# Performance work log

Measured on AMD Instinct MI355X. Metric: run time of the kernel, lower is better.

Reference implementation:

```python
import math
import jax, jax.numpy as jnp
import numpy as np

DIM = 1024
QK_DIM = 200
HIDDEN = 2 * DIM  # expansion_factor = 2
N = 8192


def setup_inputs() -> dict:
    key = jax.random.key(0)
    ks = jax.random.split(key, 8)
    s = 0.02
    return {
        "x": jax.random.normal(ks[0], (N, DIM), dtype=jnp.float32),
        "W_hidden": jax.random.normal(ks[1], (DIM, 2 * HIDDEN), dtype=jnp.float32) * s,
        "b_hidden": jnp.zeros((2 * HIDDEN,), dtype=jnp.float32),
        "W_qk": jax.random.normal(ks[2], (DIM, QK_DIM), dtype=jnp.float32) * s,
        "b_qk": jnp.zeros((QK_DIM,), dtype=jnp.float32),
        "gamma": 1.0 + jax.random.normal(ks[3], (2, QK_DIM), dtype=jnp.float32) * s,
        "beta": jnp.zeros((2, QK_DIM), dtype=jnp.float32),
        "W_out": jax.random.normal(ks[4], (HIDDEN, DIM), dtype=jnp.float32) * s,
        "b_out": jnp.zeros((DIM,), dtype=jnp.float32),
    }


def reference(x, W_hidden, b_hidden, W_qk, b_qk, gamma, beta, W_out, b_out):
    # to_hidden: Linear(dim -> 2*hidden) + SiLU, then chunk into v, gate
    hid = jax.nn.silu(x @ W_hidden + b_hidden)        # [N, 2H]
    v, gate = jnp.split(hid, 2, axis=-1)              # [N, H] each
    # to_qk: Linear(dim -> qk_dim) + SiLU
    qk = jax.nn.silu(x @ W_qk + b_qk)                 # [N, qk]
    # OffsetScale (heads=2): per-head affine on the shared qk
    q = qk * gamma[0] + beta[0]                       # [N, qk]
    k = qk * gamma[1] + beta[1]                       # [N, qk]
    # scores scaled by sqrt(dim) (module uses self.dim, not qk_dim)
    sim = (q @ k.T) * (1.0 / math.sqrt(x.shape[-1]))  # [N, N]
    # ReLU-squared attention (no softmax); dropout=0.0 -> identity
    attn = jnp.square(jax.nn.relu(sim))
    out = attn @ v                                    # [N, H]
    out = out * gate
    out = out @ W_out + b_out                         # [N, dim]
    # add_residual=True in this module multiplies by x
    return out * x
```

## Files before the change

### kernel.cpp

```cpp
#include <hip/hip_runtime.h>
#include <stdint.h>


typedef __bf16 bf16x8 __attribute__((ext_vector_type(8)));
typedef float f32x4 __attribute__((ext_vector_type(4)));

__device__ __forceinline__ uint16_t f2bf(float f) {
  uint32_t u = __builtin_bit_cast(uint32_t, f);
  u += 0x7fffu + ((u >> 16) & 1u);
  return (uint16_t)(u >> 16);
}
__device__ __forceinline__ float silu_f(float s) {
  return s / (1.f + __expf(-s));
}

__device__ __forceinline__ void gload16(const void* g, void* l) {
  __builtin_amdgcn_global_load_lds(
      (__attribute__((address_space(1))) void*)const_cast<void*>(g),
      (__attribute__((address_space(3))) void*)l, 16, 0, 0);
}


__global__ void cast_to_bf16(const float* __restrict__ in, uint16_t* __restrict__ out, int n4) {
  int i = blockIdx.x * blockDim.x + threadIdx.x;
  if (i < n4) {
    float4 f = ((const float4*)in)[i];
    ushort4 o;
    o.x = f2bf(f.x); o.y = f2bf(f.y); o.z = f2bf(f.z); o.w = f2bf(f.w);
    ((ushort4*)out)[i] = o;
  }
}

__global__ void transpose_cast_pad(const float* __restrict__ in, uint16_t* __restrict__ out,
                                   int R, int C, int Cp) {
  __shared__ float tile[32][33];
  int cb = blockIdx.x * 32;
  int rb = blockIdx.y * 32;
  int tx = threadIdx.x;
  int ty = threadIdx.y;
#pragma unroll
  for (int i = 0; i < 4; ++i) {
    int r = rb + ty + i * 8;
    int c = cb + tx;
    tile[ty + i * 8][tx] = (c < C) ? in[(size_t)r * C + c] : 0.f;
  }
  __syncthreads();
#pragma unroll
  for (int i = 0; i < 4; ++i) {
    int c = cb + ty + i * 8;
    if (c < Cp) out[(size_t)c * R + rb + tx] = f2bf(tile[tx][ty + i * 8]);
  }
}


struct EpiParams {
  const float* bias;
  const float* bias2;
  const float* g0;
  const float* b0;
  const float* g1;
  const float* b1;
  const uint16_t* gate;
  const float* x;
  uint16_t* o16a;
  uint16_t* o16b;
  uint16_t* oq;
  uint16_t* ok;
  float* o32;
};

#define TILE128(T_, B_, BS_)                                                   \
  do {                                                                         \
    const uint16_t* base_ = SH + (B_) * 8192;                                  \
    const int kp_ = (((T_) + 3) & (NT - 1)) * 32;                              \
    uint16_t* sd_ = SH + (BS_) * 8192 + wave * 512;                            \
    gload16(gA0 + kp_, sd_);                                                   \
    gload16(gA1 + kp_, sd_ + 2048);                                            \
    gload16(gB0 + kp_, sd_ + 4096);                                            \
    gload16(gB1 + kp_, sd_ + 6144);                                            \
    bf16x8 a_[4], b_[4];                                                       \
    _Pragma("unroll") for (int j = 0; j < 4; ++j)                              \
        b_[j] = *(const bf16x8*)(base_ + rdB + j * 512);                       \
    _Pragma("unroll") for (int i = 0; i < 4; ++i)                              \
        a_[i] = *(const bf16x8*)(base_ + rdA + i * 512);                       \
    __builtin_amdgcn_s_setprio(1);                                             \
    _Pragma("unroll") for (int i = 0; i < 4; ++i)                              \
      _Pragma("unroll") for (int j = 0; j < 4; ++j)                            \
          acc[i][j] = __builtin_amdgcn_mfma_f32_16x16x32_bf16(                 \
              a_[i], b_[j], acc[i][j], 0, 0, 0);                               \
    __builtin_amdgcn_s_setprio(0);                                             \
    asm volatile("s_waitcnt vmcnt(8)" ::: "memory");                           \
    __builtin_amdgcn_sched_barrier(0);                                         \
    __builtin_amdgcn_s_barrier();                                              \
    __builtin_amdgcn_sched_barrier(0);                                         \
  } while (0)

#define RING_LOOP128()                                                         \
  do {                                                                         \
    _Pragma("unroll") for (int s_ = 0; s_ < 3; ++s_) {                         \
      uint16_t* d_ = SH + s_ * 8192 + wave * 512;                              \
      gload16(gA0 + s_ * 32, d_);                                              \
      gload16(gA1 + s_ * 32, d_ + 2048);                                       \
      gload16(gB0 + s_ * 32, d_ + 4096);                                       \
      gload16(gB1 + s_ * 32, d_ + 6144);                                       \
    }                                                                          \
    asm volatile("s_waitcnt vmcnt(8)" ::: "memory");                           \
    __builtin_amdgcn_sched_barrier(0);                                         \
    __builtin_amdgcn_s_barrier();                                              \
    __builtin_amdgcn_sched_barrier(0);                                         \
    for (int t0_ = 0; t0_ < NT; t0_ += 4) {                                    \
      TILE128(t0_ + 0, 0, 3);                                                  \
      TILE128(t0_ + 1, 1, 0);                                                  \
      TILE128(t0_ + 2, 2, 1);                                                  \
      TILE128(t0_ + 3, 3, 2);                                                  \
    }                                                                          \
    asm volatile("s_waitcnt vmcnt(0)" ::: "memory");                           \
    __builtin_amdgcn_sched_barrier(0);                                         \
    __syncthreads();                                                           \
  } while (0)

__global__ __launch_bounds__(256, 2) void k_hidqk(
    const uint16_t* __restrict__ A, const uint16_t* __restrict__ Bt, EpiParams p) {
  __shared__ __align__(16) uint16_t SH[32768];

  const int tid = threadIdx.x;
  const int lane = tid & 63;
  const int wave = tid >> 6;
  const int wr = (wave >> 1) * 64;
  const int wc = (wave & 1) * 64;
  const int m0 = blockIdx.y * 128;
  const int n0 = blockIdx.x * 128;
  const int lda = 1024, ldb = 1024;
  const int NT = 32;

  f32x4 acc[4][4] = {};

  const int fr = lane & 15;
  const int rg = lane >> 4;
  const int swz = (rg ^ ((fr >> 1) & 3)) * 8;
  const int rdA = (wr + fr) * 32 + swz;
  const int rdB = 4096 + (wc + fr) * 32 + swz;

  const int srow = lane >> 2;
  const int sk = ((lane & 3) ^ ((lane >> 3) & 3)) * 8;
  const uint16_t* gA0 = A + (size_t)(m0 + wave * 16 + srow) * lda + sk;
  const uint16_t* gA1 = gA0 + (size_t)64 * lda;
  const uint16_t* gB0 = Bt + (size_t)(n0 + wave * 16 + srow) * ldb + sk;
  const uint16_t* gB1 = gB0 + (size_t)64 * ldb;

  RING_LOOP128();

  if (n0 < 2048) {
    uint16_t* ar = SH + wave * 2048;
    const int lrow = lane >> 3;
    const int mc = (lane & 7) * 8;
#pragma unroll
    for (int j = 0; j < 4; ++j) {
      const float bc = p.bias[n0 + wc + j * 16 + fr];
#pragma unroll
      for (int i = 0; i < 4; ++i)
#pragma unroll
        for (int r = 0; r < 4; ++r)
          ar[fr * 72 + i * 16 + rg * 4 + r] = f2bf(silu_f(acc[i][j][r] + bc));
#pragma unroll
      for (int rr = 0; rr < 2; ++rr) {
        bf16x8 v = *(const bf16x8*)(ar + (rr * 8 + lrow) * 72 + mc);
        *(bf16x8*)(p.o16a + (size_t)(n0 + wc + j * 16 + rr * 8 + lrow) * 8192 + m0 + wr + mc) = v;
      }
    }
  } else if (n0 < 4096) {
    uint16_t* ar = SH + wave * 2048;
    const int lrow = lane >> 3;
    const int nc = (lane & 7) * 8;
    float bc[4];
#pragma unroll
    for (int j = 0; j < 4; ++j) bc[j] = p.bias[n0 + wc + j * 16 + fr];
#pragma unroll
    for (int i = 0; i < 4; ++i) {
#pragma unroll
      for (int j = 0; j < 4; ++j)
#pragma unroll
        for (int r = 0; r < 4; ++r)
          ar[(rg * 4 + r) * 72 + j * 16 + fr] = f2bf(silu_f(acc[i][j][r] + bc[j]));
#pragma unroll
      for (int rr = 0; rr < 2; ++rr) {
        bf16x8 v = *(const bf16x8*)(ar + (rr * 8 + lrow) * 72 + nc);
        *(bf16x8*)(p.o16b + (size_t)(m0 + wr + i * 16 + rr * 8 + lrow) * 2048 + (n0 - 2048) + wc + nc) = v;
      }
    }
  } else {
#pragma unroll
    for (int i = 0; i < 4; ++i) {
#pragma unroll
      for (int j = 0; j < 4; ++j) {
        const int row = m0 + wr + i * 16 + rg * 4;
        const int qc = n0 + wc + j * 16 + fr - 4096;
#pragma unroll
        for (int r = 0; r < 4; ++r) {
          float qv = 0.f, kv = 0.f;
          if (qc < 200) {
            float s = silu_f(acc[i][j][r] + p.bias2[qc]);
            qv = s * p.g0[qc] + p.b0[qc];
            kv = s * p.g1[qc] + p.b1[qc];
          }
          p.oq[(size_t)(row + r) * 256 + qc] = f2bf(qv);
          p.ok[(size_t)(row + r) * 256 + qc] = f2bf(kv);
        }
      }
    }
  }
}

__global__ __launch_bounds__(256, 2) void k_attn(
    const uint16_t* __restrict__ Q,
    const uint16_t* __restrict__ Kt,
    uint16_t* __restrict__ attn) {
  __shared__ __align__(16) uint16_t SH[32768];

  const int tid = threadIdx.x;
  const int lane = tid & 63;
  const int wave = tid >> 6;
  const int wr = (wave >> 1) * 64;
  const int wc = (wave & 1) * 64;
  const int m0 = blockIdx.y * 128;
  const int n0 = blockIdx.x * 128;
  const int lda = 256, ldb = 256;
  const int NT = 8;

  f32x4 acc[4][4] = {};

  const int fr = lane & 15;
  const int rg = lane >> 4;
  const int swz = (rg ^ ((fr >> 1) & 3)) * 8;
  const int rdA = (wr + fr) * 32 + swz;
  const int rdB = 4096 + (wc + fr) * 32 + swz;

  const int srow = lane >> 2;
  const int sk = ((lane & 3) ^ ((lane >> 3) & 3)) * 8;
  const uint16_t* gA0 = Q + (size_t)(m0 + wave * 16 + srow) * lda + sk;
  const uint16_t* gA1 = gA0 + (size_t)64 * lda;
  const uint16_t* gB0 = Kt + (size_t)(n0 + wave * 16 + srow) * ldb + sk;
  const uint16_t* gB1 = gB0 + (size_t)64 * ldb;

  RING_LOOP128();

#pragma unroll
  for (int i = 0; i < 4; ++i) {
    uint16_t* sl = SH + wave * 4096 + (i & 1) * 2048;
#pragma unroll
    for (int j = 0; j < 4; ++j)
#pragma unroll
      for (int r = 0; r < 4; ++r) {
        float s = fmaxf(acc[i][j][r] * 0.03125f, 0.f);
        sl[(rg * 4 + r) * 72 + j * 16 + fr] = f2bf(s * s);
      }
    const int row = lane >> 2;
    const int c0 = (lane & 3) * 16;
    bf16x8 v0 = *(const bf16x8*)(sl + row * 72 + c0);
    bf16x8 v1 = *(const bf16x8*)(sl + row * 72 + c0 + 8);
    uint16_t* dst = attn + (size_t)(m0 + wr + i * 16 + row) * 8192 + (n0 + wc + c0);
    *(bf16x8*)(dst) = v0;
    *(bf16x8*)(dst + 8) = v1;
  }
}

__global__ __launch_bounds__(512, 2) void k_pv(
    const uint16_t* __restrict__ A, int lda,
    const uint16_t* __restrict__ Bt, int ldb,
    int K, int nx, EpiParams p) {
  __shared__ __align__(16) uint16_t SH[65536];

  const int id = blockIdx.x;
  const int bx = (id >> 3) % nx;
  const int by = (id & 7) + 8 * (id / (8 * nx));
  const int m0 = by * 256;
  const int n0 = bx * 256;

  const int tid = threadIdx.x;
  const int lane = tid & 63;
  const int wave = tid >> 6;
  const int wrM = (wave >> 2) * 128;
  const int wcN = (wave & 3) * 64;

  const int fr = lane & 15;
  const int rg = lane >> 4;
  const int swz = (rg ^ ((fr >> 1) & 3)) * 8;

  const int rdA = (wrM + fr) * 32 + swz;
  const int rdB = 8192 + (wcN + fr) * 32 + swz;

  const int srow = lane >> 2;
  const int sk = ((lane & 3) ^ ((lane >> 3) & 3)) * 8;
  const uint16_t* gA0 = A + (size_t)(m0 + wave * 16 + srow) * lda + sk;
  const uint16_t* gA1 = gA0 + (size_t)128 * lda;
  const uint16_t* gB0 = Bt + (size_t)(n0 + wave * 16 + srow) * ldb + sk;
  const uint16_t* gB1 = gB0 + (size_t)128 * ldb;

  f32x4 acc[8][4] = {};
  const int NT = K >> 5;

  for (int s = 0; s < 3; ++s) {
    const int ko = s * 32;
    uint16_t* d = SH + s * 16384 + wave * 512;
    gload16(gA0 + ko, d);
    gload16(gA1 + ko, d + 4096);
    gload16(gB0 + ko, d + 8192);
    gload16(gB1 + ko, d + 12288);
  }
  asm volatile("s_waitcnt vmcnt(8)" ::: "memory");
  __builtin_amdgcn_sched_barrier(0);
  __builtin_amdgcn_s_barrier();
  __builtin_amdgcn_sched_barrier(0);

#define PV_TILE(T_, B_, BS_)                                                   \
  do {                                                                         \
    const uint16_t* bA_ = SH + (B_) * 16384;                                   \
    const int kp_ = (((T_) + 3) & (NT - 1)) * 32;                              \
    uint16_t* sd_ = SH + (BS_) * 16384 + wave * 512;                           \
    gload16(gA0 + kp_, sd_);                                                   \
    gload16(gA1 + kp_, sd_ + 4096);                                            \
    gload16(gB0 + kp_, sd_ + 8192);                                            \
    gload16(gB1 + kp_, sd_ + 12288);                                           \
    bf16x8 aq[8], bq[4];                                                       \
    _Pragma("unroll") for (int j = 0; j < 4; ++j)                              \
        bq[j] = *(const bf16x8*)(bA_ + rdB + j * 512);                         \
    _Pragma("unroll") for (int i = 0; i < 8; ++i)                              \
        aq[i] = *(const bf16x8*)(bA_ + rdA + i * 512);                         \
    __builtin_amdgcn_s_setprio(1);                                             \
    _Pragma("unroll") for (int i = 0; i < 8; ++i)                              \
      _Pragma("unroll") for (int j = 0; j < 4; ++j)                            \
          acc[i][j] = __builtin_amdgcn_mfma_f32_16x16x32_bf16(                 \
              aq[i], bq[j], acc[i][j], 0, 0, 0);                               \
    __builtin_amdgcn_s_setprio(0);                                             \
    asm volatile("s_waitcnt vmcnt(8)" ::: "memory");                           \
    __builtin_amdgcn_sched_barrier(0);                                         \
    __builtin_amdgcn_s_barrier();                                              \
    __builtin_amdgcn_sched_barrier(0);                                         \
  } while (0)

  for (int t0 = 0; t0 < NT; t0 += 4) {
    PV_TILE(t0 + 0, 0, 3);
    PV_TILE(t0 + 1, 1, 0);
    PV_TILE(t0 + 2, 2, 1);
    PV_TILE(t0 + 3, 3, 2);
  }
#undef PV_TILE

  asm volatile("s_waitcnt vmcnt(0)" ::: "memory");
  __builtin_amdgcn_sched_barrier(0);
  __builtin_amdgcn_s_barrier();
  __builtin_amdgcn_sched_barrier(0);

  uint16_t* ar = SH + wave * 2048;
  const int lrow = lane >> 3;
  const int nc = (lane & 7) * 8;
#pragma unroll
  for (int i = 0; i < 8; ++i) {
#pragma unroll
    for (int j = 0; j < 4; ++j)
#pragma unroll
      for (int r = 0; r < 4; ++r)
        ar[(rg * 4 + r) * 72 + j * 16 + fr] = f2bf(acc[i][j][r]);
#pragma unroll
    for (int rr = 0; rr < 2; ++rr) {
      const size_t base = (size_t)(m0 + wrM + i * 16 + rr * 8 + lrow) * 2048 + n0 + wcN + nc;
      bf16x8 v = *(const bf16x8*)(ar + (rr * 8 + lrow) * 72 + nc);
      bf16x8 g = *(const bf16x8*)(p.gate + base);
      bf16x8 o;
#pragma unroll
      for (int e = 0; e < 8; ++e) o[e] = (__bf16)((float)v[e] * (float)g[e]);
      *(bf16x8*)(p.o16a + base) = o;
    }
  }
}

__global__ __launch_bounds__(256, 2) void k_final(
    const uint16_t* __restrict__ A,
    const uint16_t* __restrict__ Bt, EpiParams p) {
  __shared__ __align__(16) uint16_t SH[32768];

  const int tid = threadIdx.x;
  const int lane = tid & 63;
  const int wave = tid >> 6;
  const int wr = (wave >> 1) * 64;
  const int wc = (wave & 1) * 64;
  const int m0 = blockIdx.y * 128;
  const int n0 = blockIdx.x * 128;
  const int lda = 2048, ldb = 2048;
  const int NT = 64;

  f32x4 acc[4][4] = {};

  const int fr = lane & 15;
  const int rg = lane >> 4;
  const int swz = (rg ^ ((fr >> 1) & 3)) * 8;
  const int rdA = (wr + fr) * 32 + swz;
  const int rdB = 4096 + (wc + fr) * 32 + swz;

  const int srow = lane >> 2;
  const int sk = ((lane & 3) ^ ((lane >> 3) & 3)) * 8;
  const uint16_t* gA0 = A + (size_t)(m0 + wave * 16 + srow) * lda + sk;
  const uint16_t* gA1 = gA0 + (size_t)64 * lda;
  const uint16_t* gB0 = Bt + (size_t)(n0 + wave * 16 + srow) * ldb + sk;
  const uint16_t* gB1 = gB0 + (size_t)64 * ldb;

  RING_LOOP128();

#pragma unroll
  for (int i = 0; i < 4; ++i) {
#pragma unroll
    for (int j = 0; j < 4; ++j) {
      const int row = m0 + wr + i * 16 + rg * 4;
      const int col = n0 + wc + j * 16 + fr;
      const float bc = p.bias[col];
#pragma unroll
      for (int r = 0; r < 4; ++r) {
        size_t idx = (size_t)(row + r) * 1024 + col;
        p.o32[idx] = (acc[i][j][r] + bc) * p.x[idx];
      }
    }
  }
}


extern "C" void kernel_launch(void* const* d_in, const int* in_sizes, int n_in,
                              void* d_out, int out_size, void* d_ws, size_t ws_size,
                              hipStream_t stream) {
  const float* x        = (const float*)d_in[0];
  const float* W_hidden = (const float*)d_in[1];
  const float* b_hidden = (const float*)d_in[2];
  const float* W_qk     = (const float*)d_in[3];
  const float* b_qk     = (const float*)d_in[4];
  const float* gamma    = (const float*)d_in[5];
  const float* beta     = (const float*)d_in[6];
  const float* W_out    = (const float*)d_in[7];
  const float* b_out    = (const float*)d_in[8];
  float* out = (float*)d_out;

  const bool fullM = ws_size >= (236ull << 20);
  const size_t region0 = fullM ? (128ull << 20) : (64ull << 20);

  char* base = (char*)d_ws;
  uint16_t* xb    = (uint16_t*)(base);
  uint16_t* WhT   = (uint16_t*)(base + (16ull << 20));
  uint16_t* WqkT  = (uint16_t*)(base + (24ull << 20));
  uint16_t* attnB = (uint16_t*)(base);
  char* tail = base + region0;
  uint16_t* WoT   = (uint16_t*)(tail);
  uint16_t* q     = (uint16_t*)(tail + (4ull << 20));
  uint16_t* kk    = (uint16_t*)(tail + (8ull << 20));
  uint16_t* vT    = (uint16_t*)(tail + (12ull << 20));
  uint16_t* gate  = (uint16_t*)(tail + (44ull << 20));
  uint16_t* out2g = (uint16_t*)(tail + (76ull << 20));
  (void)in_sizes; (void)n_in; (void)out_size;

  cast_to_bf16<<<(8192 * 1024 / 4) / 256, 256, 0, stream>>>(x, xb, 8192 * 1024 / 4);
  transpose_cast_pad<<<dim3(4096 / 32, 1024 / 32), dim3(32, 8), 0, stream>>>(W_hidden, WhT, 1024, 4096, 4096);
  transpose_cast_pad<<<dim3(256 / 32, 1024 / 32), dim3(32, 8), 0, stream>>>(W_qk, WqkT, 1024, 200, 256);
  transpose_cast_pad<<<dim3(1024 / 32, 2048 / 32), dim3(32, 8), 0, stream>>>(W_out, WoT, 2048, 1024, 1024);

  {
    EpiParams p{};
    p.bias = b_hidden; p.bias2 = b_qk;
    p.g0 = gamma; p.b0 = beta; p.g1 = gamma + 200; p.b1 = beta + 200;
    p.o16a = vT; p.o16b = gate; p.oq = q; p.ok = kk;
    k_hidqk<<<dim3(34, 64), 256, 0, stream>>>(xb, WhT, p);
  }

  if (fullM) {
    k_attn<<<dim3(64, 64), 256, 0, stream>>>(q, kk, attnB);
    {
      EpiParams p{};
      p.gate = gate; p.o16a = out2g;
      k_pv<<<dim3(8 * 32), 512, 0, stream>>>(attnB, 8192, vT, 8192, 8192, 8, p);
    }
  } else {
    for (int s = 0; s < 2; ++s) {
      k_attn<<<dim3(64, 32), 256, 0, stream>>>(q + (size_t)s * 4096 * 256, kk, attnB);
      {
        EpiParams p{};
        p.gate = gate + (size_t)s * 4096 * 2048;
        p.o16a = out2g + (size_t)s * 4096 * 2048;
        k_pv<<<dim3(8 * 16), 512, 0, stream>>>(attnB, 8192, vT, 8192, 8192, 8, p);
      }
    }
  }

  {
    EpiParams p{};
    p.bias = b_out; p.x = x; p.o32 = out;
    k_final<<<dim3(8, 64), 256, 0, stream>>>(out2g, WoT, p);
  }
}
```

Baseline: 570.5 us.

## Halve PV tile M to 128 and double-buffer LDS fragment reads in registers

```diff
diff --git a/kernel.cpp b/kernel.cpp
--- a/kernel.cpp
+++ b/kernel.cpp
@@ -268,18 +268,18 @@
     const uint16_t* __restrict__ A, int lda,
     const uint16_t* __restrict__ Bt, int ldb,
     int K, int nx, EpiParams p) {
-  __shared__ __align__(16) uint16_t SH[65536];
+  __shared__ __align__(16) uint16_t SH[49152];
 
   const int id = blockIdx.x;
   const int bx = (id >> 3) % nx;
   const int by = (id & 7) + 8 * (id / (8 * nx));
-  const int m0 = by * 256;
+  const int m0 = by * 128;
   const int n0 = bx * 256;
 
   const int tid = threadIdx.x;
   const int lane = tid & 63;
   const int wave = tid >> 6;
-  const int wrM = (wave >> 2) * 128;
+  const int wrM = (wave >> 2) * 64;
   const int wcN = (wave & 3) * 64;
 
   const int fr = lane & 15;
@@ -287,64 +287,67 @@
   const int swz = (rg ^ ((fr >> 1) & 3)) * 8;
 
   const int rdA = (wrM + fr) * 32 + swz;
-  const int rdB = 8192 + (wcN + fr) * 32 + swz;
+  const int rdB = 4096 + (wcN + fr) * 32 + swz;
 
   const int srow = lane >> 2;
   const int sk = ((lane & 3) ^ ((lane >> 3) & 3)) * 8;
   const uint16_t* gA0 = A + (size_t)(m0 + wave * 16 + srow) * lda + sk;
-  const uint16_t* gA1 = gA0 + (size_t)128 * lda;
-  const uint16_t* gB0 = Bt + (size_t)(n0 + wave * 16 + srow) * ldb + sk;
-  const uint16_t* gB1 = gB0 + (size_t)128 * ldb;
-
-  f32x4 acc[8][4] = {};
+  const uint16_t* gB0 = Bt + (size_t)(n0 + wave * 32 + srow) * ldb + sk;
+  const uint16_t* gB1 = gB0 + (size_t)16 * ldb;
+
+  f32x4 acc[4][4] = {};
   const int NT = K >> 5;
 
   for (int s = 0; s < 3; ++s) {
     const int ko = s * 32;
-    uint16_t* d = SH + s * 16384 + wave * 512;
-    gload16(gA0 + ko, d);
-    gload16(gA1 + ko, d + 4096);
-    gload16(gB0 + ko, d + 8192);
-    gload16(gB1 + ko, d + 12288);
-  }
-  asm volatile("s_waitcnt vmcnt(8)" ::: "memory");
+    uint16_t* d = SH + s * 12288;
+    gload16(gA0 + ko, d + wave * 512);
+    gload16(gB0 + ko, d + 4096 + wave * 1024);
+    gload16(gB1 + ko, d + 4096 + wave * 1024 + 512);
+  }
+  asm volatile("s_waitcnt vmcnt(3)" ::: "memory");
   __builtin_amdgcn_sched_barrier(0);
   __builtin_amdgcn_s_barrier();
   __builtin_amdgcn_sched_barrier(0);
 
-#define PV_TILE(T_, B_, BS_)                                                   \
+  bf16x8 fa0[4], fb0[4], fa1[4], fb1[4];
+#pragma unroll
+  for (int j = 0; j < 4; ++j) fb0[j] = *(const bf16x8*)(SH + rdB + j * 512);
+#pragma unroll
+  for (int i = 0; i < 4; ++i) fa0[i] = *(const bf16x8*)(SH + rdA + i * 512);
+
+#define PV_T(T_, RS_, WS_, CA_, CB_, NA_, NB_)                                 \
   do {                                                                         \
-    const uint16_t* bA_ = SH + (B_) * 16384;                                   \
     const int kp_ = (((T_) + 3) & (NT - 1)) * 32;                              \
-    uint16_t* sd_ = SH + (BS_) * 16384 + wave * 512;                           \
-    gload16(gA0 + kp_, sd_);                                                   \
-    gload16(gA1 + kp_, sd_ + 4096);                                            \
-    gload16(gB0 + kp_, sd_ + 8192);                                            \
-    gload16(gB1 + kp_, sd_ + 12288);                                           \
-    bf16x8 aq[8], bq[4];                                                       \
+    uint16_t* sd_ = SH + (WS_) * 12288;                                        \
+    gload16(gA0 + kp_, sd_ + wave * 512);                                      \
+    gload16(gB0 + kp_, sd_ + 4096 + wave * 1024);                              \
+    gload16(gB1 + kp_, sd_ + 4096 + wave * 1024 + 512);                        \
+    const uint16_t* rb_ = SH + (RS_) * 12288;                                  \
     _Pragma("unroll") for (int j = 0; j < 4; ++j)                              \
-        bq[j] = *(const bf16x8*)(bA_ + rdB + j * 512);                         \
-    _Pragma("unroll") for (int i = 0; i < 8; ++i)                              \
-        aq[i] = *(const bf16x8*)(bA_ + rdA + i * 512);                         \
+        NB_[j] = *(const bf16x8*)(rb_ + rdB + j * 512);                        \
+    _Pragma("unroll") for (int i = 0; i < 4; ++i)                              \
+        NA_[i] = *(const bf16x8*)(rb_ + rdA + i * 512);                        \
+    __builtin_amdgcn_sched_barrier(0);                                         \
     __builtin_amdgcn_s_setprio(1);                                             \
-    _Pragma("unroll") for (int i = 0; i < 8; ++i)                              \
+    _Pragma("unroll") for (int i = 0; i < 4; ++i)                              \
       _Pragma("unroll") for (int j = 0; j < 4; ++j)                            \
           acc[i][j] = __builtin_amdgcn_mfma_f32_16x16x32_bf16(                 \
-              aq[i], bq[j], acc[i][j], 0, 0, 0);                               \
+              CA_[i], CB_[j], acc[i][j], 0, 0, 0);                             \
     __builtin_amdgcn_s_setprio(0);                                             \
-    asm volatile("s_waitcnt vmcnt(8)" ::: "memory");                           \
+    asm volatile("s_waitcnt vmcnt(3)" ::: "memory");                           \
     __builtin_amdgcn_sched_barrier(0);                                         \
     __builtin_amdgcn_s_barrier();                                              \
     __builtin_amdgcn_sched_barrier(0);                                         \
   } while (0)
 
   for (int t0 = 0; t0 < NT; t0 += 4) {
-    PV_TILE(t0 + 0, 0, 3);
-    PV_TILE(t0 + 1, 1, 0);
-    PV_TILE(t0 + 2, 2, 1);
-    PV_TILE(t0 + 3, 3, 2);
-  }
-#undef PV_TILE
+    PV_T(t0 + 0, 1, 3, fa0, fb0, fa1, fb1);
+    PV_T(t0 + 1, 2, 0, fa1, fb1, fa0, fb0);
+    PV_T(t0 + 2, 3, 1, fa0, fb0, fa1, fb1);
+    PV_T(t0 + 3, 0, 2, fa1, fb1, fa0, fb0);
+  }
+#undef PV_T
 
   asm volatile("s_waitcnt vmcnt(0)" ::: "memory");
   __builtin_amdgcn_sched_barrier(0);
@@ -355,7 +358,7 @@
   const int lrow = lane >> 3;
   const int nc = (lane & 7) * 8;
 #pragma unroll
-  for (int i = 0; i < 8; ++i) {
+  for (int i = 0; i < 4; ++i) {
 #pragma unroll
     for (int j = 0; j < 4; ++j)
 #pragma unroll
@@ -472,7 +475,7 @@
     {
       EpiParams p{};
       p.gate = gate; p.o16a = out2g;
-      k_pv<<<dim3(8 * 32), 512, 0, stream>>>(attnB, 8192, vT, 8192, 8192, 8, p);
+      k_pv<<<dim3(8 * 64), 512, 0, stream>>>(attnB, 8192, vT, 8192, 8192, 8, p);
     }
   } else {
     for (int s = 0; s < 2; ++s) {
@@ -481,7 +484,7 @@
         EpiParams p{};
         p.gate = gate + (size_t)s * 4096 * 2048;
         p.o16a = out2g + (size_t)s * 4096 * 2048;
-        k_pv<<<dim3(8 * 16), 512, 0, stream>>>(attnB, 8192, vT, 8192, 8192, 8, p);
+        k_pv<<<dim3(8 * 32), 512, 0, stream>>>(attnB, 8192, vT, 8192, 8192, 8, p);
       }
     }
   }
```

Result: slower. 604.3 us (+5.9%).

## Split PV GEMM over K halves into partial buffers and add a sum-gate kernel

Applied to the files above, without the earlier changes.

```diff
diff --git a/kernel.cpp b/kernel.cpp
--- a/kernel.cpp
+++ b/kernel.cpp
@@ -49,6 +49,21 @@
   for (int i = 0; i < 4; ++i) {
     int c = cb + ty + i * 8;
     if (c < Cp) out[(size_t)c * R + rb + tx] = f2bf(tile[tx][ty + i * 8]);
+  }
+}
+
+__global__ void k_sum(uint16_t* __restrict__ P0, const uint16_t* __restrict__ P1,
+                      const uint16_t* __restrict__ g, int n8) {
+  int i = blockIdx.x * blockDim.x + threadIdx.x;
+  if (i < n8) {
+    bf16x8 a = ((const bf16x8*)P0)[i];
+    bf16x8 b = ((const bf16x8*)P1)[i];
+    bf16x8 gg = ((const bf16x8*)g)[i];
+    bf16x8 o;
+#pragma unroll
+    for (int e = 0; e < 8; ++e)
+      o[e] = (__bf16)(((float)a[e] + (float)b[e]) * (float)gg[e]);
+    ((bf16x8*)P0)[i] = o;
   }
 }
 
@@ -265,16 +280,19 @@
 }
 
 __global__ __launch_bounds__(512, 2) void k_pv(
-    const uint16_t* __restrict__ A, int lda,
-    const uint16_t* __restrict__ Bt, int ldb,
-    int K, int nx, EpiParams p) {
+    const uint16_t* __restrict__ A,
+    const uint16_t* __restrict__ Bt,
+    uint16_t* __restrict__ P0,
+    uint16_t* __restrict__ P1) {
   __shared__ __align__(16) uint16_t SH[65536];
 
   const int id = blockIdx.x;
-  const int bx = (id >> 3) % nx;
-  const int by = (id & 7) + 8 * (id / (8 * nx));
+  const int bx = id & 7;
+  const int kh = (id >> 3) & 1;
+  const int by = id >> 4;
   const int m0 = by * 256;
   const int n0 = bx * 256;
+  const int kv0 = kh * 4096;
 
   const int tid = threadIdx.x;
   const int lane = tid & 63;
@@ -291,13 +309,13 @@
 
   const int srow = lane >> 2;
   const int sk = ((lane & 3) ^ ((lane >> 3) & 3)) * 8;
-  const uint16_t* gA0 = A + (size_t)(m0 + wave * 16 + srow) * lda + sk;
-  const uint16_t* gA1 = gA0 + (size_t)128 * lda;
-  const uint16_t* gB0 = Bt + (size_t)(n0 + wave * 16 + srow) * ldb + sk;
-  const uint16_t* gB1 = gB0 + (size_t)128 * ldb;
+  const uint16_t* gA0 = A + (size_t)(m0 + wave * 16 + srow) * 8192 + kv0 + sk;
+  const uint16_t* gA1 = gA0 + (size_t)128 * 8192;
+  const uint16_t* gB0 = Bt + (size_t)(n0 + wave * 16 + srow) * 8192 + kv0 + sk;
+  const uint16_t* gB1 = gB0 + (size_t)128 * 8192;
 
   f32x4 acc[8][4] = {};
-  const int NT = K >> 5;
+  const int NT = 128;
 
   for (int s = 0; s < 3; ++s) {
     const int ko = s * 32;
@@ -351,6 +369,7 @@
   __builtin_amdgcn_s_barrier();
   __builtin_amdgcn_sched_barrier(0);
 
+  uint16_t* dst = kh ? P1 : P0;
   uint16_t* ar = SH + wave * 2048;
   const int lrow = lane >> 3;
   const int nc = (lane & 7) * 8;
@@ -365,11 +384,7 @@
     for (int rr = 0; rr < 2; ++rr) {
       const size_t base = (size_t)(m0 + wrM + i * 16 + rr * 8 + lrow) * 2048 + n0 + wcN + nc;
       bf16x8 v = *(const bf16x8*)(ar + (rr * 8 + lrow) * 72 + nc);
-      bf16x8 g = *(const bf16x8*)(p.gate + base);
-      bf16x8 o;
-#pragma unroll
-      for (int e = 0; e < 8; ++e) o[e] = (__bf16)((float)v[e] * (float)g[e]);
-      *(bf16x8*)(p.o16a + base) = o;
+      *(bf16x8*)(dst + base) = v;
     }
   }
 }
@@ -437,22 +452,21 @@
   const float* b_out    = (const float*)d_in[8];
   float* out = (float*)d_out;
 
-  const bool fullM = ws_size >= (236ull << 20);
-  const size_t region0 = fullM ? (128ull << 20) : (64ull << 20);
-
   char* base = (char*)d_ws;
   uint16_t* xb    = (uint16_t*)(base);
   uint16_t* WhT   = (uint16_t*)(base + (16ull << 20));
   uint16_t* WqkT  = (uint16_t*)(base + (24ull << 20));
   uint16_t* attnB = (uint16_t*)(base);
-  char* tail = base + region0;
+  char* tail = base + (64ull << 20);
   uint16_t* WoT   = (uint16_t*)(tail);
   uint16_t* q     = (uint16_t*)(tail + (4ull << 20));
   uint16_t* kk    = (uint16_t*)(tail + (8ull << 20));
   uint16_t* vT    = (uint16_t*)(tail + (12ull << 20));
   uint16_t* gate  = (uint16_t*)(tail + (44ull << 20));
   uint16_t* out2g = (uint16_t*)(tail + (76ull << 20));
-  (void)in_sizes; (void)n_in; (void)out_size;
+  (void)in_sizes; (void)n_in; (void)out_size; (void)ws_size;
+
+  const size_t PH = 4096ull * 2048;
 
   cast_to_bf16<<<(8192 * 1024 / 4) / 256, 256, 0, stream>>>(x, xb, 8192 * 1024 / 4);
   transpose_cast_pad<<<dim3(4096 / 32, 1024 / 32), dim3(32, 8), 0, stream>>>(W_hidden, WhT, 1024, 4096, 4096);
@@ -467,28 +481,20 @@
     k_hidqk<<<dim3(34, 64), 256, 0, stream>>>(xb, WhT, p);
   }
 
-  if (fullM) {
-    k_attn<<<dim3(64, 64), 256, 0, stream>>>(q, kk, attnB);
-    {
-      EpiParams p{};
-      p.gate = gate; p.o16a = out2g;
-      k_pv<<<dim3(8 * 32), 512, 0, stream>>>(attnB, 8192, vT, 8192, 8192, 8, p);
-    }
-  } else {
-    for (int s = 0; s < 2; ++s) {
-      k_attn<<<dim3(64, 32), 256, 0, stream>>>(q + (size_t)s * 4096 * 256, kk, attnB);
-      {
-        EpiParams p{};
-        p.gate = gate + (size_t)s * 4096 * 2048;
-        p.o16a = out2g + (size_t)s * 4096 * 2048;
-        k_pv<<<dim3(8 * 16), 512, 0, stream>>>(attnB, 8192, vT, 8192, 8192, 8, p);
-      }
-    }
-  }
-
-  {
+  for (int s = 0; s < 2; ++s) {
+    k_attn<<<dim3(64, 32), 256, 0, stream>>>(q + (size_t)s * 4096 * 256, kk, attnB);
+
+    uint16_t* Pa = out2g + (size_t)s * PH;
+    uint16_t* Pb = out2g + (size_t)(1 - s) * PH;
+    k_pv<<<dim3(256), 512, 0, stream>>>(attnB, vT, Pa, Pb);
+
+    k_sum<<<dim3((int)(PH / 8 / 256)), 256, 0, stream>>>(
+        Pa, Pb, gate + (size_t)s * PH, (int)(PH / 8));
+
     EpiParams p{};
-    p.bias = b_out; p.x = x; p.o32 = out;
-    k_final<<<dim3(8, 64), 256, 0, stream>>>(out2g, WoT, p);
-  }
-}
+    p.bias = b_out;
+    p.x = x + (size_t)s * 4096 * 1024;
+    p.o32 = out + (size_t)s * 4096 * 1024;
+    k_final<<<dim3(8, 32), 256, 0, stream>>>(Pa, WoT, p);
+  }
+}
```

Measured after the change: 653.5 us. +14.5%, slower.
